# Performance work log

Hardware: AMD Instinct MI355X
Metric: run time of the kernel (lower is better)

Reference implementation:

```python
import jax, jax.numpy as jnp
import numpy as np

P = 0.15  # masking probability (init kwarg p)

def setup_inputs() -> dict:
    key = jax.random.key(0)
    k1, k2 = jax.random.split(key)
    B, T, D = 64, 2048, 256
    x = jax.random.normal(k1, (B, T, D), dtype=jnp.float32)
    rand = jax.random.uniform(k2, (B, T), dtype=jnp.float32)
    return {"x": x, "rand": rand}

def reference(x, rand):
    # keep token where rand > p (same predicate as torch.rand > p)
    B, T, D = x.shape
    keep = rand > P                                  # [B,T] bool
    cs = jnp.cumsum(keep.astype(jnp.int32), axis=1)  # inclusive count of kept tokens
    l = cs[:, -1:]                                   # [B,1] kept per row
    # kept token at position t goes to T - l + rank, rank = cs-1; dropped tokens -> T (out of bounds, dropped)
    dest = jnp.where(keep, T - l + cs - 1, T)        # [B,T]
    out = jnp.zeros_like(x)
    out = out.at[jnp.arange(B)[:, None], dest].set(x, mode='drop')
    return out
```

## Files before the change

kernel.cpp:

```cpp
#include <hip/hip_runtime.h>


#define P_DROP 0.15f

typedef float f32x4 __attribute__((ext_vector_type(4)));

__global__ __launch_bounds__(256)
void seqmask_scan_kernel(const float* __restrict__ rand,
                         int* __restrict__ l_out,
                         int* __restrict__ src,
                         int T) {
    const int b    = blockIdx.x;
    const int tid  = threadIdx.x;
    const int wave = tid >> 6;
    const int lane = tid & 63;
    const float* r = rand + (size_t)b * T + tid * 8;

    f32x4 r0 = *reinterpret_cast<const f32x4*>(r);
    f32x4 r1 = *reinterpret_cast<const f32x4*>(r + 4);

    int keep[8];
    keep[0] = r0.x > P_DROP; keep[1] = r0.y > P_DROP;
    keep[2] = r0.z > P_DROP; keep[3] = r0.w > P_DROP;
    keep[4] = r1.x > P_DROP; keep[5] = r1.y > P_DROP;
    keep[6] = r1.z > P_DROP; keep[7] = r1.w > P_DROP;

    int cnt = 0;
#pragma unroll
    for (int i = 0; i < 8; ++i) cnt += keep[i];

    int inc = cnt;
#pragma unroll
    for (int off = 1; off < 64; off <<= 1) {
        int n = __shfl_up(inc, off, 64);
        if (lane >= off) inc += n;
    }

    __shared__ int wsum[4];
    if (lane == 63) wsum[wave] = inc;
    __syncthreads();

    int wexcl = 0;
#pragma unroll
    for (int w = 0; w < 4; ++w) wexcl += (w < wave) ? wsum[w] : 0;
    const int total = wsum[0] + wsum[1] + wsum[2] + wsum[3];
    if (tid == 0) l_out[b] = total;

    int pos = wexcl + inc - cnt;
    int* sb = src + (size_t)b * T;
#pragma unroll
    for (int i = 0; i < 8; ++i) {
        if (keep[i]) {
            sb[pos] = tid * 8 + i;
            ++pos;
        }
    }
}

__global__ __launch_bounds__(256)
void seqmask_gather_kernel(const float* __restrict__ x,
                           const int* __restrict__ l_arr,
                           const int* __restrict__ src,
                           float* __restrict__ out,
                           int T, int D) {
    const int row  = blockIdx.x * 4 + (threadIdx.x >> 6);
    const int lane = threadIdx.x & 63;
    const int b    = row >> 11;
    const int j    = row & (T - 1);

    const int l = l_arr[b];
    const int q = j - (T - l);

    f32x4 v = (f32x4)(0.f, 0.f, 0.f, 0.f);
    if (q >= 0) {
        const int st = src[(size_t)b * T + q];
        v = *reinterpret_cast<const f32x4*>(
                x + ((size_t)b * T + st) * D + lane * 4);
    }
    *reinterpret_cast<f32x4*>(out + (size_t)row * D + lane * 4) = v;
}

extern "C" void kernel_launch(void* const* d_in, const int* in_sizes, int n_in,
                              void* d_out, int out_size, void* d_ws, size_t ws_size,
                              hipStream_t stream) {
    const float* x    = (const float*)d_in[0];
    const float* rand = (const float*)d_in[1];
    float* out        = (float*)d_out;

    const int T  = 2048;
    const int BT = in_sizes[1];
    const int D  = in_sizes[0] / BT;

    int* l_arr = (int*)d_ws;
    int* src   = (int*)((char*)d_ws + 256);

    seqmask_scan_kernel<<<BT / T, 256, 0, stream>>>(rand, l_arr, src, T);
    seqmask_gather_kernel<<<BT / 4, 256, 0, stream>>>(x, l_arr, src, out, T, D);
}
```

Baseline: 45.96 us.

## Fuse scan and gather into one kernel with per-block redundant scan in LDS

Merges the two kernels into one. Each block recomputes the full-row keep scan for its batch row into a shared-memory index map, then gathers 16 output rows. This removes the second launch and the global round trip of the src and l arrays. In exchange, every batch row's rand is read and scanned 128 times, and the block's gather waits behind a scan and two barriers. T and D are now hardcoded.

```diff
diff --git a/kernel.cpp b/kernel.cpp
--- a/kernel.cpp
+++ b/kernel.cpp
@@ -6,16 +6,20 @@
 typedef float f32x4 __attribute__((ext_vector_type(4)));
 
 __global__ __launch_bounds__(256)
-void seqmask_scan_kernel(const float* __restrict__ rand,
-                         int* __restrict__ l_out,
-                         int* __restrict__ src,
-                         int T) {
-    const int b    = blockIdx.x;
+void seqmask_fused_kernel(const float* __restrict__ x,
+                          const float* __restrict__ rand,
+                          float* __restrict__ out) {
+    const int T = 2048, D = 256;
+    const int b    = blockIdx.x >> 7;
+    const int j0   = (blockIdx.x & 127) << 4;
     const int tid  = threadIdx.x;
     const int wave = tid >> 6;
     const int lane = tid & 63;
+
+    __shared__ int smap[2048];
+    __shared__ int wsum[4];
+
     const float* r = rand + (size_t)b * T + tid * 8;
-
     f32x4 r0 = *reinterpret_cast<const f32x4*>(r);
     f32x4 r1 = *reinterpret_cast<const f32x4*>(r + 4);
 
@@ -35,49 +39,33 @@
         int n = __shfl_up(inc, off, 64);
         if (lane >= off) inc += n;
     }
-
-    __shared__ int wsum[4];
     if (lane == 63) wsum[wave] = inc;
     __syncthreads();
 
     int wexcl = 0;
 #pragma unroll
     for (int w = 0; w < 4; ++w) wexcl += (w < wave) ? wsum[w] : 0;
-    const int total = wsum[0] + wsum[1] + wsum[2] + wsum[3];
-    if (tid == 0) l_out[b] = total;
+    const int l = wsum[0] + wsum[1] + wsum[2] + wsum[3];
 
     int pos = wexcl + inc - cnt;
-    int* sb = src + (size_t)b * T;
 #pragma unroll
     for (int i = 0; i < 8; ++i) {
-        if (keep[i]) {
-            sb[pos] = tid * 8 + i;
-            ++pos;
+        if (keep[i]) smap[pos++] = tid * 8 + i;
+    }
+    __syncthreads();
+
+    const size_t xb = (size_t)b * T * D;
+#pragma unroll
+    for (int rr = 0; rr < 4; ++rr) {
+        const int j = j0 + wave * 4 + rr;
+        const int q = j - (T - l);
+        f32x4 v = (f32x4)(0.f, 0.f, 0.f, 0.f);
+        if (q >= 0) {
+            const int st = smap[q];
+            v = *reinterpret_cast<const f32x4*>(x + xb + (size_t)st * D + lane * 4);
         }
+        *reinterpret_cast<f32x4*>(out + xb + (size_t)j * D + lane * 4) = v;
     }
-}
-
-__global__ __launch_bounds__(256)
-void seqmask_gather_kernel(const float* __restrict__ x,
-                           const int* __restrict__ l_arr,
-                           const int* __restrict__ src,
-                           float* __restrict__ out,
-                           int T, int D) {
-    const int row  = blockIdx.x * 4 + (threadIdx.x >> 6);
-    const int lane = threadIdx.x & 63;
-    const int b    = row >> 11;
-    const int j    = row & (T - 1);
-
-    const int l = l_arr[b];
-    const int q = j - (T - l);
-
-    f32x4 v = (f32x4)(0.f, 0.f, 0.f, 0.f);
-    if (q >= 0) {
-        const int st = src[(size_t)b * T + q];
-        v = *reinterpret_cast<const f32x4*>(
-                x + ((size_t)b * T + st) * D + lane * 4);
-    }
-    *reinterpret_cast<f32x4*>(out + (size_t)row * D + lane * 4) = v;
 }
 
 extern "C" void kernel_launch(void* const* d_in, const int* in_sizes, int n_in,
@@ -87,13 +75,6 @@
     const float* rand = (const float*)d_in[1];
     float* out        = (float*)d_out;
 
-    const int T  = 2048;
     const int BT = in_sizes[1];
-    const int D  = in_sizes[0] / BT;
-
-    int* l_arr = (int*)d_ws;
-    int* src   = (int*)((char*)d_ws + 256);
-
-    seqmask_scan_kernel<<<BT / T, 256, 0, stream>>>(rand, l_arr, src, T);
-    seqmask_gather_kernel<<<BT / 4, 256, 0, stream>>>(x, l_arr, src, out, T, D);
+    seqmask_fused_kernel<<<BT / 16, 256, 0, stream>>>(x, rand, out);
 }
```

New measurement: 42.90 us. 6.7% less time.
